# Kernel optimization log

Hardware: AMD Instinct MI355X
Metric: run time of the kernel (lower is better)

The kernel has to match this reference:

```python
import jax, jax.numpy as jnp
import numpy as np

N = 50000      # nodes
E = 800000     # edges
F_IN = 10      # node_feat_dim
H = 64         # hidden
ED = 3         # edge_dim
L = 3          # num_layers
EPS_LN = 1e-5


def _layernorm(x, g, b):
    mu = jnp.mean(x, axis=-1, keepdims=True)
    var = jnp.mean((x - mu) ** 2, axis=-1, keepdims=True)
    return (x - mu) * jax.lax.rsqrt(var + EPS_LN) * g + b


def setup_inputs() -> dict:
    key = jax.random.key(0)
    ks = jax.random.split(key, 20)
    x = jax.random.normal(ks[0], (N, F_IN), dtype=jnp.float32)
    edge_index = jax.random.randint(ks[1], (2, E), 0, N, dtype=jnp.int32)
    edge_attr = jax.random.uniform(ks[2], (E, ED), dtype=jnp.float32)

    def lin(k, fan_in, shape):
        return jax.random.normal(k, shape, dtype=jnp.float32) / np.sqrt(fan_in)

    params = {
        "Wp": lin(ks[3], F_IN, (F_IN, H)),
        "bp": jnp.zeros((H,), jnp.float32),
        # per-layer stacked params, leading dim L
        "ew1": lin(ks[4], ED, (L, ED, 16)),
        "eb1": jnp.zeros((L, 16), jnp.float32),
        "ew2": lin(ks[5], 16, (L, 16, 1)),
        "eb2": jnp.zeros((L, 1), jnp.float32),
        "nw": lin(ks[6], 2 * H, (L, 2 * H, H)),
        "nb": jnp.zeros((L, H), jnp.float32),
        "ln_g": jnp.ones((L, H), jnp.float32),
        "ln_b": jnp.zeros((L, H), jnp.float32),
        "hw1": lin(ks[7], H, (H, H // 2)),
        "hb1": jnp.zeros((H // 2,), jnp.float32),
        "hw2": lin(ks[8], H // 2, (H // 2, 1)),
        "hb2": jnp.zeros((1,), jnp.float32),
    }
    return {"x": x, "edge_index": edge_index, "edge_attr": edge_attr, **params}


def reference(x, edge_index, edge_attr, Wp, bp, ew1, eb1, ew2, eb2,
              nw, nb, ln_g, ln_b, hw1, hb1, hw2, hb2):
    src, dst = edge_index[0], edge_index[1]
    h = jax.nn.relu(x @ Wp + bp)                       # (N, H)
    for l in range(L):
        # edge MLP -> sigmoid weight per edge, shape (E, 1)
        ew = jax.nn.sigmoid(jax.nn.relu(edge_attr @ ew1[l] + eb1[l]) @ ew2[l] + eb2[l])
        msg = h[src] * ew                              # (E, H) gather + scale
        agg = jax.ops.segment_sum(msg, dst, num_segments=N)   # (N, H)
        cnt = jax.ops.segment_sum(ew, dst, num_segments=N)    # (N, 1)
        agg = agg / jnp.maximum(cnt, 1e-12)
        upd = jax.nn.relu(jnp.concatenate([h, agg], axis=1) @ nw[l] + nb[l])
        h = _layernorm(h + upd, ln_g[l], ln_b[l])
    return jax.nn.relu(h @ hw1 + hb1) @ hw2 + hb2      # (N, 1) logits
```

## Files before the change

### kernel.cpp

```cpp
#include <hip/hip_runtime.h>
#include <math.h>

#define N_NODES 50000
#define N_EDGES 800000
#define N_STRIPS 3125
#define N_BUCKETS 196
#define CAP_B 6144
#define CHUNK_A 2048
#define PROJ_BLOCKS 12500

typedef __attribute__((ext_vector_type(8))) short bf16x8;
typedef __attribute__((ext_vector_type(4))) float f32x4;
typedef __attribute__((ext_vector_type(2))) float f32x2;

__device__ __forceinline__ unsigned short f2bf(float f) {
  unsigned int u = __float_as_uint(f);
  u += 0x7FFFu + ((u >> 16) & 1u);
  return (unsigned short)(u >> 16);
}
__device__ __forceinline__ float bf2f(unsigned short s) {
  return __uint_as_float(((unsigned int)s) << 16);
}
__device__ __forceinline__ unsigned char f2fp8(float f) {
  return (unsigned char)(__builtin_amdgcn_cvt_pk_fp8_f32(f, f, 0, false) & 0xFF);
}

__global__ __launch_bounds__(256) void k_proj(const float* __restrict__ x,
                                              const float* __restrict__ Wp,
                                              const float* __restrict__ bp,
                                              unsigned short* __restrict__ hb,
                                              unsigned char* __restrict__ h8,
                                              int* __restrict__ bcur,
                                              int* __restrict__ ocnt,
                                              int* __restrict__ ocur) {
  int bid = blockIdx.x;
  if (bid == PROJ_BLOCKS) {
    if (threadIdx.x < N_BUCKETS) bcur[threadIdx.x] = threadIdx.x * CAP_B;
    if (threadIdx.x < 8) { ocnt[threadIdx.x] = 0; ocur[threadIdx.x] = 0; }
    return;
  }
  int idx = bid * 256 + threadIdx.x;
  int n = idx >> 6, j = idx & 63;
  float acc = bp[j];
#pragma unroll
  for (int k = 0; k < 10; k++) acc += x[n * 10 + k] * Wp[k * 64 + j];
  float r = fmaxf(acc, 0.f);
  hb[n * 64 + j] = f2bf(r);
  h8[n * 64 + j] = f2fp8(r);
}

__global__ __launch_bounds__(256) void k_fillA(const int* __restrict__ ei,
                                               const float* __restrict__ ea,
                                               const float* __restrict__ ew1,
                                               const float* __restrict__ eb1,
                                               const float* __restrict__ ew2,
                                               const float* __restrict__ eb2,
                                               int* __restrict__ bcur,
                                               uint2* __restrict__ buf1) {
  __shared__ int lcnt[N_BUCKETS];
  __shared__ int gb[N_BUCKETS];
  for (int i = threadIdx.x; i < N_BUCKETS; i += 256) lcnt[i] = 0;
  __syncthreads();
  int base = blockIdx.x * CHUNK_A;
  uint2 rec[CHUNK_A / 256];
  int bk[CHUNK_A / 256], rk[CHUNK_A / 256];
#pragma unroll
  for (int k = 0; k < CHUNK_A / 256; k++) {
    int e = base + k * 256 + threadIdx.x;
    bk[k] = -1;
    if (e < N_EDGES) {
      int s = ei[e];
      int d = ei[N_EDGES + e];
      float a0 = ea[e * 3 + 0], a1 = ea[e * 3 + 1], a2 = ea[e * 3 + 2];
      int q[3];
#pragma unroll
      for (int l = 0; l < 3; l++) {
        float z = eb2[l];
#pragma unroll
        for (int t = 0; t < 16; t++) {
          float hd = a0 * ew1[l * 48 + t] + a1 * ew1[l * 48 + 16 + t] +
                     a2 * ew1[l * 48 + 32 + t] + eb1[l * 16 + t];
          z += fmaxf(hd, 0.f) * ew2[l * 16 + t];
        }
        float w = 1.f / (1.f + __expf(-z));
        q[l] = __float2int_rn(w * 8191.f);
      }
      unsigned int dl = (unsigned int)(d & 255);
      rec[k].x = (unsigned int)s | ((unsigned int)q[0] << 17) | ((dl & 3u) << 30);
      rec[k].y = (unsigned int)q[1] | ((unsigned int)q[2] << 13) | ((dl >> 2) << 26);
      int b = d >> 8;
      bk[k] = b;
      rk[k] = atomicAdd(&lcnt[b], 1);
    }
  }
  __syncthreads();
  if (threadIdx.x < N_BUCKETS) {
    int c = lcnt[threadIdx.x];
    gb[threadIdx.x] = c ? atomicAdd(&bcur[threadIdx.x], c) : 0;
  }
  __syncthreads();
#pragma unroll
  for (int k = 0; k < CHUNK_A / 256; k++)
    if (bk[k] >= 0) buf1[gb[bk[k]] + rk[k]] = rec[k];
}

__global__ __launch_bounds__(256) void k_fillB(const uint2* __restrict__ buf1,
                                               const int* __restrict__ bcur,
                                               uint2* __restrict__ csr,
                                               int* __restrict__ aoffs,
                                               int* __restrict__ adeg,
                                               int* __restrict__ ocnt) {
  __shared__ int lhist[256];
  __shared__ int lscan[256];
  __shared__ int lcls[8];
  int b = blockIdx.x;
  int t = threadIdx.x;
  int segbase = b * CAP_B;
  int cnt = bcur[b] - segbase;
  lhist[t] = 0;
  if (t < 8) lcls[t] = 0;
  __syncthreads();
  for (int i = t; i < cnt; i += 256) {
    uint2 rec = buf1[segbase + i];
    int dl = (int)((rec.x >> 30) | (((rec.y >> 26) & 63u) << 2));
    atomicAdd(&lhist[dl], 1);
  }
  __syncthreads();
  int v = lhist[t];
  lscan[t] = v;
  __syncthreads();
#pragma unroll
  for (int off = 1; off < 256; off <<= 1) {
    int u = (t >= off) ? lscan[t - off] : 0;
    __syncthreads();
    lscan[t] += u;
    __syncthreads();
  }
  int excl = lscan[t] - v;
  int nid = b * 256 + t;
  if (nid < N_NODES) {
    aoffs[nid] = segbase + excl;
    adeg[nid] = v;
    atomicAdd(&lcls[min(v >> 2, 7)], 1);
  }
  __syncthreads();
  if (t < 8 && lcls[t]) atomicAdd(&ocnt[t], lcls[t]);
  lhist[t] = segbase + excl;
  __syncthreads();
  for (int i = t; i < cnt; i += 256) {
    uint2 rec = buf1[segbase + i];
    int dl = (int)((rec.x >> 30) | (((rec.y >> 26) & 63u) << 2));
    int pos = atomicAdd(&lhist[dl], 1);
    csr[pos] = rec;
  }
}

__global__ __launch_bounds__(256) void k_order(const int* __restrict__ adeg,
                                               const int* __restrict__ ocnt,
                                               int* __restrict__ ocur,
                                               int* __restrict__ order) {
  __shared__ int lc[8], gb[8];
  int t = threadIdx.x;
  int nid = blockIdx.x * 256 + t;
  if (t < 8) lc[t] = 0;
  __syncthreads();
  int cls = 0, rank = 0;
  bool act = nid < N_NODES;
  if (act) {
    cls = min(adeg[nid] >> 2, 7);
    rank = atomicAdd(&lc[cls], 1);
  }
  __syncthreads();
  if (t < 8) {
    int base = 0;
#pragma unroll
    for (int c = 0; c < 8; c++) base += (c < t) ? ocnt[c] : 0;
    int c = lc[t];
    gb[t] = base + (c ? atomicAdd(&ocur[t], c) : 0);
  }
  __syncthreads();
  if (act) order[gb[cls] + rank] = nid;
}

template <int LI>
__device__ __forceinline__ float decw(uint2 c) {
  unsigned int q = (LI == 0) ? ((c.x >> 17) & 0x1FFFu)
                 : (LI == 1) ? (c.y & 0x1FFFu)
                             : ((c.y >> 13) & 0x1FFFu);
  return (float)q * (1.f / 8191.f);
}

template <int LI>
__global__ __launch_bounds__(256, 8) void k_agg(const uint2* __restrict__ csr,
                                                const int* __restrict__ aoffs,
                                                const int* __restrict__ adeg,
                                                const int* __restrict__ order,
                                                const unsigned char* __restrict__ h8in,
                                                unsigned short* __restrict__ ab) {
  int lane = threadIdx.x & 63;
  int sub = lane >> 3;
  int jj = lane & 7;
  int gw = (blockIdx.x * 256 + threadIdx.x) >> 6;
  int idx = gw * 8 + sub;
  bool active = idx < N_NODES;
  int n = active ? order[idx] : 0;
  int start = active ? aoffs[n] : 0;
  int d = active ? adeg[n] : 0;
  const uint2* hrow = (const uint2*)h8in;
  float a0 = 0.f, a1 = 0.f, a2 = 0.f, a3 = 0.f;
  float a4 = 0.f, a5 = 0.f, a6 = 0.f, a7 = 0.f, ws = 0.f;
  int i = 0;
  for (; i + 4 <= d; i += 4) {
    uint2 c0 = csr[start + i + 0];
    uint2 c1 = csr[start + i + 1];
    uint2 c2 = csr[start + i + 2];
    uint2 c3 = csr[start + i + 3];
    uint2 g0 = hrow[(c0.x & 0x1FFFFu) * 8 + jj];
    uint2 g1 = hrow[(c1.x & 0x1FFFFu) * 8 + jj];
    uint2 g2 = hrow[(c2.x & 0x1FFFFu) * 8 + jj];
    uint2 g3 = hrow[(c3.x & 0x1FFFFu) * 8 + jj];
    float w0 = decw<LI>(c0), w1 = decw<LI>(c1), w2 = decw<LI>(c2), w3 = decw<LI>(c3);
#pragma unroll
    for (int k = 0; k < 4; k++) {
      uint2 g = (k == 0) ? g0 : (k == 1) ? g1 : (k == 2) ? g2 : g3;
      float w = (k == 0) ? w0 : (k == 1) ? w1 : (k == 2) ? w2 : w3;
      f32x2 p01 = __builtin_amdgcn_cvt_pk_f32_fp8(g.x, false);
      f32x2 p23 = __builtin_amdgcn_cvt_pk_f32_fp8(g.x, true);
      f32x2 p45 = __builtin_amdgcn_cvt_pk_f32_fp8(g.y, false);
      f32x2 p67 = __builtin_amdgcn_cvt_pk_f32_fp8(g.y, true);
      a0 += p01[0] * w; a1 += p01[1] * w;
      a2 += p23[0] * w; a3 += p23[1] * w;
      a4 += p45[0] * w; a5 += p45[1] * w;
      a6 += p67[0] * w; a7 += p67[1] * w;
    }
    ws += w0 + w1 + w2 + w3;
  }
  for (; i < d; ++i) {
    uint2 c = csr[start + i];
    uint2 g = hrow[(c.x & 0x1FFFFu) * 8 + jj];
    float w = decw<LI>(c);
    f32x2 p01 = __builtin_amdgcn_cvt_pk_f32_fp8(g.x, false);
    f32x2 p23 = __builtin_amdgcn_cvt_pk_f32_fp8(g.x, true);
    f32x2 p45 = __builtin_amdgcn_cvt_pk_f32_fp8(g.y, false);
    f32x2 p67 = __builtin_amdgcn_cvt_pk_f32_fp8(g.y, true);
    a0 += p01[0] * w; a1 += p01[1] * w;
    a2 += p23[0] * w; a3 += p23[1] * w;
    a4 += p45[0] * w; a5 += p45[1] * w;
    a6 += p67[0] * w; a7 += p67[1] * w;
    ws += w;
  }
  if (active) {
    float inv = 1.f / fmaxf(ws, 1e-12f);
    uint4 o;
    o.x = (unsigned int)f2bf(a0 * inv) | ((unsigned int)f2bf(a1 * inv) << 16);
    o.y = (unsigned int)f2bf(a2 * inv) | ((unsigned int)f2bf(a3 * inv) << 16);
    o.z = (unsigned int)f2bf(a4 * inv) | ((unsigned int)f2bf(a5 * inv) << 16);
    o.w = (unsigned int)f2bf(a6 * inv) | ((unsigned int)f2bf(a7 * inv) << 16);
    ((uint4*)ab)[n * 8 + jj] = o;
  }
}

template <bool HEAD>
__global__ __launch_bounds__(256) void k_mlp(const float* __restrict__ nw,
                                             const float* __restrict__ nb,
                                             const float* __restrict__ g,
                                             const float* __restrict__ b,
                                             const unsigned short* __restrict__ hb_in,
                                             const unsigned short* __restrict__ ab_in,
                                             unsigned short* __restrict__ hbout,
                                             unsigned char* __restrict__ h8out,
                                             const float* __restrict__ hw1,
                                             const float* __restrict__ hb1,
                                             const float* __restrict__ hw2,
                                             const float* __restrict__ hb2,
                                             float* __restrict__ out) {
  __shared__ unsigned short lh[4][16 * 72];
  int lane = threadIdx.x & 63;
  int n16 = lane & 15;
  int q = lane >> 4;
  int wv = threadIdx.x >> 6;
  int wid = (blockIdx.x * 256 + threadIdx.x) >> 6;
  int nwaves = gridDim.x * 4;

  bf16x8 bfr[4][4];
#pragma unroll
  for (int t = 0; t < 4; t++)
#pragma unroll
    for (int kc = 0; kc < 4; kc++) {
      bf16x8 v;
#pragma unroll
      for (int jj = 0; jj < 8; jj++) {
        int k = kc * 32 + q * 8 + jj;
        v[jj] = (short)f2bf(nw[k * 64 + t * 16 + n16]);
      }
      bfr[t][kc] = v;
    }
  bf16x8 eye[2];
#pragma unroll
  for (int p = 0; p < 2; p++) {
    bf16x8 v;
#pragma unroll
    for (int jj = 0; jj < 8; jj++)
      v[jj] = ((q * 8 + jj) == (n16 + 16 * p)) ? (short)0x3F80 : (short)0;
    eye[p] = v;
  }
  float nbv[4], gv[4], bv[4];
#pragma unroll
  for (int t = 0; t < 4; t++) {
    nbv[t] = nb[t * 16 + n16];
    gv[t] = g[t * 16 + n16];
    bv[t] = b[t * 16 + n16];
  }
  bf16x8 hfr[2][2];
  float hb1v[2], hw2v[2], hb2v = 0.f;
  if (HEAD) {
#pragma unroll
    for (int kc = 0; kc < 2; kc++)
#pragma unroll
      for (int tl = 0; tl < 2; tl++) {
        bf16x8 v;
#pragma unroll
        for (int jj = 0; jj < 8; jj++)
          v[jj] = (short)f2bf(hw1[(kc * 32 + q * 8 + jj) * 32 + tl * 16 + n16]);
        hfr[kc][tl] = v;
      }
#pragma unroll
    for (int tl = 0; tl < 2; tl++) {
      hb1v[tl] = hb1[tl * 16 + n16];
      hw2v[tl] = hw2[tl * 16 + n16];
    }
    hb2v = hb2[0];
  }

  for (int s = wid; s < N_STRIPS; s += nwaves) {
    int n0 = s * 16;
    f32x4 acc[4] = {{0.f, 0.f, 0.f, 0.f}, {0.f, 0.f, 0.f, 0.f},
                    {0.f, 0.f, 0.f, 0.f}, {0.f, 0.f, 0.f, 0.f}};
    bf16x8 afr[4];
#pragma unroll
    for (int kc = 0; kc < 4; kc++) {
      const unsigned short* base = (kc < 2) ? hb_in : ab_in;
      afr[kc] = *(const bf16x8*)(base + (size_t)(n0 + n16) * 64 + (kc & 1) * 32 + q * 8);
#pragma unroll
      for (int t = 0; t < 4; t++)
        acc[t] = __builtin_amdgcn_mfma_f32_16x16x32_bf16(afr[kc], bfr[t][kc], acc[t], 0, 0, 0);
    }
    f32x4 rres[4];
#pragma unroll
    for (int t = 0; t < 4; t++) {
      f32x4 z = {0.f, 0.f, 0.f, 0.f};
      rres[t] = __builtin_amdgcn_mfma_f32_16x16x32_bf16(afr[t >> 1], eye[t & 1], z, 0, 0, 0);
    }
    float r[4][4];
    float p[4], p2[4];
#pragma unroll
    for (int rg = 0; rg < 4; rg++) { p[rg] = 0.f; p2[rg] = 0.f; }
#pragma unroll
    for (int t = 0; t < 4; t++)
#pragma unroll
      for (int rg = 0; rg < 4; rg++) {
        float rr = rres[t][rg] + fmaxf(acc[t][rg] + nbv[t], 0.f);
        r[t][rg] = rr;
        p[rg] += rr;
        p2[rg] += rr * rr;
      }
#pragma unroll
    for (int rg = 0; rg < 4; rg++)
#pragma unroll
      for (int off = 1; off < 16; off <<= 1) {
        p[rg] += __shfl_xor(p[rg], off);
        p2[rg] += __shfl_xor(p2[rg], off);
      }
#pragma unroll
    for (int rg = 0; rg < 4; rg++) {
      float mu = p[rg] * (1.f / 64.f);
      float var = p2[rg] * (1.f / 64.f) - mu * mu;
      float rs = rsqrtf(fmaxf(var, 0.f) + 1e-5f);
      int row = n0 + q * 4 + rg;
#pragma unroll
      for (int t = 0; t < 4; t++) {
        float o = (r[t][rg] - mu) * rs * gv[t] + bv[t];
        unsigned short ob = f2bf(o);
        hbout[row * 64 + t * 16 + n16] = ob;
        h8out[row * 64 + t * 16 + n16] = f2fp8(o);
        if (HEAD) lh[wv][(q * 4 + rg) * 72 + t * 16 + n16] = ob;
      }
    }
    if (HEAD) {
      asm volatile("s_waitcnt lgkmcnt(0)" ::: "memory");
      f32x4 hacc[2] = {{0.f, 0.f, 0.f, 0.f}, {0.f, 0.f, 0.f, 0.f}};
#pragma unroll
      for (int kc = 0; kc < 2; kc++) {
        bf16x8 ha = *(const bf16x8*)&lh[wv][n16 * 72 + kc * 32 + q * 8];
#pragma unroll
        for (int tl = 0; tl < 2; tl++)
          hacc[tl] = __builtin_amdgcn_mfma_f32_16x16x32_bf16(ha, hfr[kc][tl], hacc[tl], 0, 0, 0);
      }
#pragma unroll
      for (int rg = 0; rg < 4; rg++) {
        float sres = fmaxf(hacc[0][rg] + hb1v[0], 0.f) * hw2v[0] +
                     fmaxf(hacc[1][rg] + hb1v[1], 0.f) * hw2v[1];
#pragma unroll
        for (int off = 1; off < 16; off <<= 1) sres += __shfl_xor(sres, off);
        if (n16 == 0) out[n0 + q * 4 + rg] = sres + hb2v;
      }
    }
  }
}

static inline size_t align256(size_t x) { return (x + 255) & ~size_t(255); }

extern "C" void kernel_launch(void* const* d_in, const int* in_sizes, int n_in,
                              void* d_out, int out_size, void* d_ws, size_t ws_size,
                              hipStream_t stream) {
  const float* x   = (const float*)d_in[0];
  const int*   ei  = (const int*)d_in[1];
  const float* ea  = (const float*)d_in[2];
  const float* Wp  = (const float*)d_in[3];
  const float* bp  = (const float*)d_in[4];
  const float* ew1 = (const float*)d_in[5];
  const float* eb1 = (const float*)d_in[6];
  const float* ew2 = (const float*)d_in[7];
  const float* eb2 = (const float*)d_in[8];
  const float* nw  = (const float*)d_in[9];
  const float* nb  = (const float*)d_in[10];
  const float* lng = (const float*)d_in[11];
  const float* lnb = (const float*)d_in[12];
  const float* hw1 = (const float*)d_in[13];
  const float* hb1 = (const float*)d_in[14];
  const float* hw2 = (const float*)d_in[15];
  const float* hb2 = (const float*)d_in[16];
  float* out = (float*)d_out;

  char* ws = (char*)d_ws;
  size_t off = 0;
  unsigned short* hb0  = (unsigned short*)(ws + off); off = align256(off + (size_t)N_NODES * 64 * 2);
  unsigned short* hb1b = (unsigned short*)(ws + off); off = align256(off + (size_t)N_NODES * 64 * 2);
  unsigned short* ab   = (unsigned short*)(ws + off); off = align256(off + (size_t)N_NODES * 64 * 2);
  unsigned char* h8_0  = (unsigned char*)(ws + off); off = align256(off + (size_t)N_NODES * 64);
  unsigned char* h8_1  = (unsigned char*)(ws + off); off = align256(off + (size_t)N_NODES * 64);
  uint2* csr  = (uint2*)(ws + off); off = align256(off + (size_t)N_BUCKETS * CAP_B * 8);
  uint2* buf1 = (uint2*)(ws + off); off = align256(off + (size_t)N_BUCKETS * CAP_B * 8);
  int* aoffs  = (int*)(ws + off); off = align256(off + (size_t)N_NODES * 4);
  int* adeg   = (int*)(ws + off); off = align256(off + (size_t)N_NODES * 4);
  int* order  = (int*)(ws + off); off = align256(off + (size_t)N_NODES * 4);
  int* bcur   = (int*)(ws + off); off = align256(off + 1024);
  int* ocnt   = (int*)(ws + off); off = align256(off + 256);
  int* ocur   = (int*)(ws + off); off = align256(off + 256);

  k_proj<<<PROJ_BLOCKS + 1, 256, 0, stream>>>(x, Wp, bp, hb0, h8_0, bcur, ocnt, ocur);
  k_fillA<<<(N_EDGES + CHUNK_A - 1) / CHUNK_A, 256, 0, stream>>>(ei, ea, ew1, eb1, ew2, eb2, bcur, buf1);
  k_fillB<<<N_BUCKETS, 256, 0, stream>>>(buf1, bcur, csr, aoffs, adeg, ocnt);
  k_order<<<N_BUCKETS, 256, 0, stream>>>(adeg, ocnt, ocur, order);

  const int aggGrid = (N_NODES + 31) / 32;
  const int mlpGrid = 392;

  k_agg<0><<<aggGrid, 256, 0, stream>>>(csr, aoffs, adeg, order, h8_0, ab);
  k_mlp<false><<<mlpGrid, 256, 0, stream>>>(nw + 0 * 8192, nb + 0 * 64, lng + 0 * 64, lnb + 0 * 64,
                                            hb0, ab, hb1b, h8_1, hw1, hb1, hw2, hb2, out);
  k_agg<1><<<aggGrid, 256, 0, stream>>>(csr, aoffs, adeg, order, h8_1, ab);
  k_mlp<false><<<mlpGrid, 256, 0, stream>>>(nw + 1 * 8192, nb + 1 * 64, lng + 1 * 64, lnb + 1 * 64,
                                            hb1b, ab, hb0, h8_0, hw1, hb1, hw2, hb2, out);
  k_agg<2><<<aggGrid, 256, 0, stream>>>(csr, aoffs, adeg, order, h8_0, ab);
  k_mlp<true><<<mlpGrid, 256, 0, stream>>>(nw + 2 * 8192, nb + 2 * 64, lng + 2 * 64, lnb + 2 * 64,
                                           hb0, ab, hb1b, h8_1, hw1, hb1, hw2, hb2, out);
}
```

Before: 223.3 us.

## Fuse projection into edge bucketing, order per bucket, and use nontemporal loads

Merges the node projection kernel and the edge bucketing kernel into a single launch that splits blocks by role. A memset replaces the in-kernel counter initialisation. The separate degree-ordering kernel is dropped: each bucket block now sorts its own nodes by degree class locally, so ordering is per bucket rather than global. Many loads become nontemporal to reduce cache pollution. Together this cuts the launch count by two, but the local ordering may balance the aggregation kernel less well than the global sort did.

```diff
diff --git a/kernel.cpp b/kernel.cpp
--- a/kernel.cpp
+++ b/kernel.cpp
@@ -7,6 +7,7 @@
 #define N_BUCKETS 196
 #define CAP_B 6144
 #define CHUNK_A 2048
+#define FILLA_BLOCKS 391
 #define PROJ_BLOCKS 12500
 
 typedef __attribute__((ext_vector_type(8))) short bf16x8;
@@ -24,41 +25,40 @@
 __device__ __forceinline__ unsigned char f2fp8(float f) {
   return (unsigned char)(__builtin_amdgcn_cvt_pk_fp8_f32(f, f, 0, false) & 0xFF);
 }
-
-__global__ __launch_bounds__(256) void k_proj(const float* __restrict__ x,
-                                              const float* __restrict__ Wp,
-                                              const float* __restrict__ bp,
-                                              unsigned short* __restrict__ hb,
-                                              unsigned char* __restrict__ h8,
-                                              int* __restrict__ bcur,
-                                              int* __restrict__ ocnt,
-                                              int* __restrict__ ocur) {
-  int bid = blockIdx.x;
-  if (bid == PROJ_BLOCKS) {
-    if (threadIdx.x < N_BUCKETS) bcur[threadIdx.x] = threadIdx.x * CAP_B;
-    if (threadIdx.x < 8) { ocnt[threadIdx.x] = 0; ocur[threadIdx.x] = 0; }
-    return;
-  }
-  int idx = bid * 256 + threadIdx.x;
-  int n = idx >> 6, j = idx & 63;
-  float acc = bp[j];
-#pragma unroll
-  for (int k = 0; k < 10; k++) acc += x[n * 10 + k] * Wp[k * 64 + j];
-  float r = fmaxf(acc, 0.f);
-  hb[n * 64 + j] = f2bf(r);
-  h8[n * 64 + j] = f2fp8(r);
-}
-
-__global__ __launch_bounds__(256) void k_fillA(const int* __restrict__ ei,
-                                               const float* __restrict__ ea,
-                                               const float* __restrict__ ew1,
-                                               const float* __restrict__ eb1,
-                                               const float* __restrict__ ew2,
-                                               const float* __restrict__ eb2,
-                                               int* __restrict__ bcur,
-                                               uint2* __restrict__ buf1) {
+__device__ __forceinline__ uint2 nt_load_u2(const uint2* p) {
+  unsigned long long raw = __builtin_nontemporal_load((const unsigned long long*)p);
+  uint2 r;
+  r.x = (unsigned int)raw;
+  r.y = (unsigned int)(raw >> 32);
+  return r;
+}
+
+__global__ __launch_bounds__(256) void k_pre(const int* __restrict__ ei,
+                                             const float* __restrict__ ea,
+                                             const float* __restrict__ ew1,
+                                             const float* __restrict__ eb1,
+                                             const float* __restrict__ ew2,
+                                             const float* __restrict__ eb2,
+                                             int* __restrict__ bcur,
+                                             uint2* __restrict__ buf1,
+                                             const float* __restrict__ x,
+                                             const float* __restrict__ Wp,
+                                             const float* __restrict__ bp,
+                                             unsigned short* __restrict__ hb,
+                                             unsigned char* __restrict__ h8) {
   __shared__ int lcnt[N_BUCKETS];
   __shared__ int gb[N_BUCKETS];
+  if (blockIdx.x >= FILLA_BLOCKS) {
+    int idx = (blockIdx.x - FILLA_BLOCKS) * 256 + threadIdx.x;
+    int n = idx >> 6, j = idx & 63;
+    float acc = bp[j];
+#pragma unroll
+    for (int k = 0; k < 10; k++) acc += __builtin_nontemporal_load(&x[n * 10 + k]) * Wp[k * 64 + j];
+    float r = fmaxf(acc, 0.f);
+    hb[n * 64 + j] = f2bf(r);
+    h8[n * 64 + j] = f2fp8(r);
+    return;
+  }
   for (int i = threadIdx.x; i < N_BUCKETS; i += 256) lcnt[i] = 0;
   __syncthreads();
   int base = blockIdx.x * CHUNK_A;
@@ -69,9 +69,11 @@
     int e = base + k * 256 + threadIdx.x;
     bk[k] = -1;
     if (e < N_EDGES) {
-      int s = ei[e];
-      int d = ei[N_EDGES + e];
-      float a0 = ea[e * 3 + 0], a1 = ea[e * 3 + 1], a2 = ea[e * 3 + 2];
+      int s = __builtin_nontemporal_load(&ei[e]);
+      int d = __builtin_nontemporal_load(&ei[N_EDGES + e]);
+      float a0 = __builtin_nontemporal_load(&ea[e * 3 + 0]);
+      float a1 = __builtin_nontemporal_load(&ea[e * 3 + 1]);
+      float a2 = __builtin_nontemporal_load(&ea[e * 3 + 2]);
       int q[3];
 #pragma unroll
       for (int l = 0; l < 3; l++) {
@@ -96,7 +98,7 @@
   __syncthreads();
   if (threadIdx.x < N_BUCKETS) {
     int c = lcnt[threadIdx.x];
-    gb[threadIdx.x] = c ? atomicAdd(&bcur[threadIdx.x], c) : 0;
+    gb[threadIdx.x] = threadIdx.x * CAP_B + (c ? atomicAdd(&bcur[threadIdx.x], c) : 0);
   }
   __syncthreads();
 #pragma unroll
@@ -109,19 +111,20 @@
                                                uint2* __restrict__ csr,
                                                int* __restrict__ aoffs,
                                                int* __restrict__ adeg,
-                                               int* __restrict__ ocnt) {
+                                               int* __restrict__ order) {
   __shared__ int lhist[256];
   __shared__ int lscan[256];
   __shared__ int lcls[8];
+  __shared__ int lbase[8];
   int b = blockIdx.x;
   int t = threadIdx.x;
   int segbase = b * CAP_B;
-  int cnt = bcur[b] - segbase;
+  int cnt = bcur[b];
   lhist[t] = 0;
   if (t < 8) lcls[t] = 0;
   __syncthreads();
   for (int i = t; i < cnt; i += 256) {
-    uint2 rec = buf1[segbase + i];
+    uint2 rec = nt_load_u2(&buf1[segbase + i]);
     int dl = (int)((rec.x >> 30) | (((rec.y >> 26) & 63u) << 2));
     atomicAdd(&lhist[dl], 1);
   }
@@ -138,48 +141,29 @@
   }
   int excl = lscan[t] - v;
   int nid = b * 256 + t;
-  if (nid < N_NODES) {
+  int cls = 0, rank = 0;
+  bool valid = nid < N_NODES;
+  if (valid) {
     aoffs[nid] = segbase + excl;
     adeg[nid] = v;
-    atomicAdd(&lcls[min(v >> 2, 7)], 1);
-  }
-  __syncthreads();
-  if (t < 8 && lcls[t]) atomicAdd(&ocnt[t], lcls[t]);
+    cls = min(v >> 2, 7);
+    rank = atomicAdd(&lcls[cls], 1);
+  }
+  __syncthreads();
+  if (t == 0) {
+    int acc2 = 0;
+#pragma unroll
+    for (int c = 0; c < 8; c++) { lbase[c] = acc2; acc2 += lcls[c]; }
+  }
   lhist[t] = segbase + excl;
   __syncthreads();
+  if (valid) order[b * 256 + lbase[cls] + rank] = nid;
   for (int i = t; i < cnt; i += 256) {
-    uint2 rec = buf1[segbase + i];
+    uint2 rec = nt_load_u2(&buf1[segbase + i]);
     int dl = (int)((rec.x >> 30) | (((rec.y >> 26) & 63u) << 2));
     int pos = atomicAdd(&lhist[dl], 1);
     csr[pos] = rec;
   }
-}
-
-__global__ __launch_bounds__(256) void k_order(const int* __restrict__ adeg,
-                                               const int* __restrict__ ocnt,
-                                               int* __restrict__ ocur,
-                                               int* __restrict__ order) {
-  __shared__ int lc[8], gb[8];
-  int t = threadIdx.x;
-  int nid = blockIdx.x * 256 + t;
-  if (t < 8) lc[t] = 0;
-  __syncthreads();
-  int cls = 0, rank = 0;
-  bool act = nid < N_NODES;
-  if (act) {
-    cls = min(adeg[nid] >> 2, 7);
-    rank = atomicAdd(&lc[cls], 1);
-  }
-  __syncthreads();
-  if (t < 8) {
-    int base = 0;
-#pragma unroll
-    for (int c = 0; c < 8; c++) base += (c < t) ? ocnt[c] : 0;
-    int c = lc[t];
-    gb[t] = base + (c ? atomicAdd(&ocur[t], c) : 0);
-  }
-  __syncthreads();
-  if (act) order[gb[cls] + rank] = nid;
 }
 
 template <int LI>
@@ -203,18 +187,18 @@
   int gw = (blockIdx.x * 256 + threadIdx.x) >> 6;
   int idx = gw * 8 + sub;
   bool active = idx < N_NODES;
-  int n = active ? order[idx] : 0;
-  int start = active ? aoffs[n] : 0;
-  int d = active ? adeg[n] : 0;
+  int n = active ? __builtin_nontemporal_load(&order[idx]) : 0;
+  int start = active ? __builtin_nontemporal_load(&aoffs[n]) : 0;
+  int d = active ? __builtin_nontemporal_load(&adeg[n]) : 0;
   const uint2* hrow = (const uint2*)h8in;
   float a0 = 0.f, a1 = 0.f, a2 = 0.f, a3 = 0.f;
   float a4 = 0.f, a5 = 0.f, a6 = 0.f, a7 = 0.f, ws = 0.f;
   int i = 0;
   for (; i + 4 <= d; i += 4) {
-    uint2 c0 = csr[start + i + 0];
-    uint2 c1 = csr[start + i + 1];
-    uint2 c2 = csr[start + i + 2];
-    uint2 c3 = csr[start + i + 3];
+    uint2 c0 = nt_load_u2(&csr[start + i + 0]);
+    uint2 c1 = nt_load_u2(&csr[start + i + 1]);
+    uint2 c2 = nt_load_u2(&csr[start + i + 2]);
+    uint2 c3 = nt_load_u2(&csr[start + i + 3]);
     uint2 g0 = hrow[(c0.x & 0x1FFFFu) * 8 + jj];
     uint2 g1 = hrow[(c1.x & 0x1FFFFu) * 8 + jj];
     uint2 g2 = hrow[(c2.x & 0x1FFFFu) * 8 + jj];
@@ -236,7 +220,7 @@
     ws += w0 + w1 + w2 + w3;
   }
   for (; i < d; ++i) {
-    uint2 c = csr[start + i];
+    uint2 c = nt_load_u2(&csr[start + i]);
     uint2 g = hrow[(c.x & 0x1FFFFu) * 8 + jj];
     float w = decw<LI>(c);
     f32x2 p01 = __builtin_amdgcn_cvt_pk_f32_fp8(g.x, false);
@@ -340,7 +324,8 @@
 #pragma unroll
     for (int kc = 0; kc < 4; kc++) {
       const unsigned short* base = (kc < 2) ? hb_in : ab_in;
-      afr[kc] = *(const bf16x8*)(base + (size_t)(n0 + n16) * 64 + (kc & 1) * 32 + q * 8);
+      afr[kc] = __builtin_nontemporal_load(
+          (const bf16x8*)(base + (size_t)(n0 + n16) * 64 + (kc & 1) * 32 + q * 8));
 #pragma unroll
       for (int t = 0; t < 4; t++)
         acc[t] = __builtin_amdgcn_mfma_f32_16x16x32_bf16(afr[kc], bfr[t][kc], acc[t], 0, 0, 0);
@@ -445,13 +430,11 @@
   int* adeg   = (int*)(ws + off); off = align256(off + (size_t)N_NODES * 4);
   int* order  = (int*)(ws + off); off = align256(off + (size_t)N_NODES * 4);
   int* bcur   = (int*)(ws + off); off = align256(off + 1024);
-  int* ocnt   = (int*)(ws + off); off = align256(off + 256);
-  int* ocur   = (int*)(ws + off); off = align256(off + 256);
-
-  k_proj<<<PROJ_BLOCKS + 1, 256, 0, stream>>>(x, Wp, bp, hb0, h8_0, bcur, ocnt, ocur);
-  k_fillA<<<(N_EDGES + CHUNK_A - 1) / CHUNK_A, 256, 0, stream>>>(ei, ea, ew1, eb1, ew2, eb2, bcur, buf1);
-  k_fillB<<<N_BUCKETS, 256, 0, stream>>>(buf1, bcur, csr, aoffs, adeg, ocnt);
-  k_order<<<N_BUCKETS, 256, 0, stream>>>(adeg, ocnt, ocur, order);
+
+  (void)hipMemsetAsync(bcur, 0, N_BUCKETS * 4, stream);
+  k_pre<<<FILLA_BLOCKS + PROJ_BLOCKS, 256, 0, stream>>>(ei, ea, ew1, eb1, ew2, eb2, bcur, buf1,
+                                                        x, Wp, bp, hb0, h8_0);
+  k_fillB<<<N_BUCKETS, 256, 0, stream>>>(buf1, bcur, csr, aoffs, adeg, order);
 
   const int aggGrid = (N_NODES + 31) / 32;
   const int mlpGrid = 392;
```

After: 238.7 us. 1.07x slower.
